# Kernel optimization log

Hardware: AMD Instinct MI355X
Metric: run time of the kernel (lower is better)

Reference implementation:

```python
import jax, jax.numpy as jnp
import numpy as np

V, N, K, D, H = 100000, 20000, 32, 256, 256


def setup_inputs() -> dict:
    key = jax.random.key(0)
    k1, k2, k3, k4, k5, k6 = jax.random.split(key, 6)
    return {
        "embed_table": jax.random.normal(k1, (V, D), dtype=jnp.float32),
        "node_ids": jax.random.randint(k2, (N,), 0, V, dtype=jnp.int64) if jax.config.jax_enable_x64 else jax.random.randint(k2, (N,), 0, V, dtype=jnp.int32),
        "nb_ids": jax.random.randint(k3, (N, K), 0, V, dtype=jnp.int32),
        "self_weight": jax.random.normal(k4, (D, H), dtype=jnp.float32) / np.sqrt(D),
        "nb_weight": jax.random.normal(k5, (D, H), dtype=jnp.float32) / np.sqrt(D),
        "bias": jax.random.normal(k6, (2 * H,), dtype=jnp.float32),
    }


def reference(embed_table, node_ids, nb_ids, self_weight, nb_weight, bias):
    # gather self embeddings: [N, D]
    self_attr = embed_table[node_ids]
    # gather sampled neighbor embeddings [N, K, D] and mean-pool over K
    nb_attr = jnp.mean(embed_table[nb_ids], axis=1)
    from_self = self_attr @ self_weight          # [N, H]
    from_nb = nb_attr @ nb_weight                # [N, H]
    out = jnp.concatenate((from_self, from_nb), axis=1) + bias  # concat combine
    return jax.nn.relu(out)
```

## Files before the change

kernel.cpp:

```cpp
#include <hip/hip_runtime.h>

#define VV 100000
#define NN 20000
#define KK 32
#define DD 256
#define HH 256
#define BN 16

typedef __attribute__((ext_vector_type(8))) short bf16x8;
typedef __attribute__((ext_vector_type(4))) float f32x4;
typedef __attribute__((ext_vector_type(2))) float f32x2;
typedef __attribute__((ext_vector_type(4))) uint  u32x4;
typedef __attribute__((ext_vector_type(2))) uint  u32x2;

__device__ __forceinline__ ushort f2bf(float f) {
    uint u = __float_as_uint(f);
    return (ushort)((u + 0x7FFFu + ((u >> 16) & 1u)) >> 16);
}
__device__ __forceinline__ float bf2f(ushort u) {
    return __uint_as_float(((uint)u) << 16);
}

__global__ __launch_bounds__(256) void k_conv8(
    const float* __restrict__ E, unsigned char* __restrict__ E8)
{
    const size_t i = ((size_t)blockIdx.x * 256 + threadIdx.x) * 16;
    u32x4 o;
    #pragma unroll
    for (int w = 0; w < 4; ++w) {
        const f32x4 a = __builtin_nontemporal_load((const f32x4*)&E[i + w * 4]);
        int r = 0;
        r = __builtin_amdgcn_cvt_pk_fp8_f32(a.x, a.y, r, false);
        r = __builtin_amdgcn_cvt_pk_fp8_f32(a.z, a.w, r, true);
        o[w] = (uint)r;
    }
    *(u32x4*)&E8[i] = o;
}

__global__ __launch_bounds__(256) void k_conv(
    const float* __restrict__ E, ushort* __restrict__ Eb)
{
    const size_t i = ((size_t)blockIdx.x * 256 + threadIdx.x) * 8;
    const f32x4 a = __builtin_nontemporal_load((const f32x4*)&E[i]);
    const f32x4 b = __builtin_nontemporal_load((const f32x4*)&E[i + 4]);
    bf16x8 v;
    v[0] = (short)f2bf(a.x); v[1] = (short)f2bf(a.y);
    v[2] = (short)f2bf(a.z); v[3] = (short)f2bf(a.w);
    v[4] = (short)f2bf(b.x); v[5] = (short)f2bf(b.y);
    v[6] = (short)f2bf(b.z); v[7] = (short)f2bf(b.w);
    *(bf16x8*)&Eb[i] = v;
}

__global__ __launch_bounds__(256) void k_prep_wf(
    const float* __restrict__ Ws, const float* __restrict__ Wn,
    ushort* __restrict__ WTf)
{
    __shared__ float t[256][17];
    const int tid = threadIdx.x;
    const int h   = blockIdx.y;
    const int tt  = blockIdx.x;
    const float* src = h ? Wn : Ws;
    const int h0 = tt * 16;
    const int c = tid & 15, dr = tid >> 4;
    #pragma unroll
    for (int s = 0; s < 16; ++s) {
        const int d = s * 16 + dr;
        t[d][c] = src[(size_t)d * HH + h0 + c];
    }
    __syncthreads();
    const int fl = tid & 63, w = tid >> 6;
    const int r16 = fl & 15, kg = fl >> 4;
    #pragma unroll
    for (int p = 0; p < 2; ++p) {
        const int ks = w + p * 4;
        bf16x8 v;
        #pragma unroll
        for (int e = 0; e < 8; ++e)
            v[e] = (short)f2bf(t[ks * 32 + kg * 8 + e][r16]);
        *(bf16x8*)&WTf[(((size_t)(h * 16 + tt) * 8 + ks) * 64 + fl) * 8] = v;
    }
}

__global__ __launch_bounds__(256) void k_prep_w(
    const float* __restrict__ Ws, const float* __restrict__ Wn,
    ushort* __restrict__ WT)
{
    __shared__ float t[64][65];
    const int tid = threadIdx.x;
    const float* src = (blockIdx.z == 0) ? Ws : Wn;
    ushort* dst = WT + (size_t)blockIdx.z * HH * DD;
    const int d0 = blockIdx.x * 64, h0 = blockIdx.y * 64;

    const int hl = tid & 63, dq = tid >> 6;
    #pragma unroll
    for (int i = 0; i < 16; ++i) {
        const int dl = dq * 16 + i;
        t[dl][hl] = src[(size_t)(d0 + dl) * HH + h0 + hl];
    }
    __syncthreads();
    const int dl = tid & 63, hq = tid >> 6;
    #pragma unroll
    for (int i = 0; i < 16; ++i) {
        const int h2 = hq * 16 + i;
        dst[(size_t)(h0 + h2) * DD + d0 + dl] = f2bf(t[dl][h2]);
    }
}

__global__ __launch_bounds__(256, 6) void k_gather8(
    const float*         __restrict__ Ef,
    const unsigned char* __restrict__ E8,
    const int*           __restrict__ node_ids,
    const int*           __restrict__ nb_ids,
    ushort*              __restrict__ A)
{
    const int wv   = threadIdx.x >> 6;
    const int lane = threadIdx.x & 63;
    const int sub  = lane >> 5, l31 = lane & 31;
    const int g    = blockIdx.x * 4 + wv;
    const int base = g * KK;

    const int srow = node_ids[g];
    const f32x4 s0 = *(const f32x4*)&Ef[(size_t)(uint)srow * DD + l31 * 8];
    const f32x4 s1 = *(const f32x4*)&Ef[(size_t)(uint)srow * DD + l31 * 8 + 4];

    u32x2 d[16];
    #pragma unroll
    for (int j = 0; j < 16; ++j) {
        const int rlo = nb_ids[base + 2 * j];
        const int rhi = nb_ids[base + 2 * j + 1];
        const int row = sub ? rhi : rlo;
        d[j] = *(const u32x2*)&E8[(size_t)(uint)row * DD + l31 * 8];
    }

    float acc[8];
    #pragma unroll
    for (int e = 0; e < 8; ++e) acc[e] = 0.f;
    #pragma unroll
    for (int j = 0; j < 16; ++j) {
        #pragma unroll
        for (int w = 0; w < 2; ++w) {
            const f32x2 lo = __builtin_amdgcn_cvt_pk_f32_fp8((int)d[j][w], false);
            const f32x2 hi = __builtin_amdgcn_cvt_pk_f32_fp8((int)d[j][w], true);
            acc[w * 4 + 0] += lo.x; acc[w * 4 + 1] += lo.y;
            acc[w * 4 + 2] += hi.x; acc[w * 4 + 3] += hi.y;
        }
    }
    #pragma unroll
    for (int e = 0; e < 8; ++e)
        acc[e] += __shfl_xor(acc[e], 32);

    const float inv = 1.0f / (float)KK;
    bf16x8 nv;
    #pragma unroll
    for (int e = 0; e < 8; ++e)
        nv[e] = (short)f2bf(acc[e] * inv);

    bf16x8 sv;
    sv[0] = (short)f2bf(s0.x); sv[1] = (short)f2bf(s0.y);
    sv[2] = (short)f2bf(s0.z); sv[3] = (short)f2bf(s0.w);
    sv[4] = (short)f2bf(s1.x); sv[5] = (short)f2bf(s1.y);
    sv[6] = (short)f2bf(s1.z); sv[7] = (short)f2bf(s1.w);

    const int tile = g >> 4, rr = g & 15;
    const int ks = l31 >> 2, kgw = l31 & 3;
    const size_t dst = (((size_t)(tile * 2 + sub) * 8 + ks) * 64 + kgw * 16 + rr) * 8;
    *(bf16x8*)&A[dst] = sub ? nv : sv;
}

__global__ __launch_bounds__(256, 4) void k_gemmf(
    const ushort* __restrict__ A,
    const ushort* __restrict__ WTf,
    const float*  __restrict__ bias,
    float*        __restrict__ out)
{
    const int wv   = __builtin_amdgcn_readfirstlane((int)(threadIdx.x >> 6));
    const int lane = threadIdx.x & 63;
    const int tile = blockIdx.x;
    const int half = wv >> 1, qt = wv & 1;
    const int r16 = lane & 15, kg = lane >> 4;

    bf16x8 a[8];
    #pragma unroll
    for (int ks = 0; ks < 8; ++ks)
        a[ks] = *(const bf16x8*)&A[(((size_t)(tile * 2 + half) * 8 + ks) * 64 + lane) * 8];

    f32x4 accs[8];
    #pragma unroll
    for (int ct = 0; ct < 8; ++ct) {
        const int t = qt * 8 + ct;
        f32x4 acc = {0.f, 0.f, 0.f, 0.f};
        #pragma unroll
        for (int ks = 0; ks < 8; ++ks) {
            const bf16x8 b = *(const bf16x8*)&WTf[(((size_t)(half * 16 + t) * 8 + ks) * 64 + lane) * 8];
            acc = __builtin_amdgcn_mfma_f32_16x16x32_bf16(a[ks], b, acc, 0, 0, 0);
        }
        accs[ct] = acc;
    }

    #pragma unroll
    for (int ct = 0; ct < 8; ++ct) {
        const int cglob = half * HH + (qt * 8 + ct) * 16 + r16;
        const float bv = bias[cglob];
        #pragma unroll
        for (int r = 0; r < 4; ++r) {
            const float v = accs[ct][r] + bv;
            out[(size_t)(tile * 16 + kg * 4 + r) * (2 * HH) + cglob] = v > 0.f ? v : 0.f;
        }
    }
}

template<int EBF16>
__global__ __launch_bounds__(256, 4) void k_fused(
    const float*  __restrict__ Ef,
    const ushort* __restrict__ Eb,
    const int*    __restrict__ node_ids,
    const int*    __restrict__ nb_ids,
    const ushort* __restrict__ WT,
    const float*  __restrict__ bias,
    float*        __restrict__ out)
{
    __shared__ ushort As[BN][DD];
    __shared__ ushort An[BN][DD];
    const int tid  = threadIdx.x;
    const int wave = tid >> 6;
    const int lane = tid & 63;
    const int g0   = blockIdx.x * BN;

    if (EBF16) {
        const int sub = lane >> 5;
        const int l31 = lane & 31;
        const uint boff = (uint)l31 * 16;
        for (int n = wave; n < BN; n += 4) {
            const int g = g0 + n;
            const int base = g * KK;
            const uint swz = ((uint)(n & 7)) << 4;
            const int srow = node_ids[g];
            const bf16x8 sv = *(const bf16x8*)&Eb[((size_t)(uint)srow << 8) + l31 * 8];
            bf16x8 r[16];
            #pragma unroll
            for (int j = 0; j < 16; ++j) {
                const int rlo = nb_ids[base + 2 * j];
                const int rhi = nb_ids[base + 2 * j + 1];
                const int row = sub ? rhi : rlo;
                r[j] = *(const bf16x8*)&Eb[((size_t)(uint)row << 8) + l31 * 8];
            }
            float acc[8];
            #pragma unroll
            for (int e = 0; e < 8; ++e) acc[e] = 0.f;
            #pragma unroll
            for (int j = 0; j < 16; ++j) {
                #pragma unroll
                for (int e = 0; e < 8; ++e)
                    acc[e] += bf2f((ushort)r[j][e]);
            }
            #pragma unroll
            for (int e = 0; e < 8; ++e)
                acc[e] += __shfl_xor(acc[e], 32);
            const float inv = 1.0f / (float)KK;
            bf16x8 nv;
            #pragma unroll
            for (int e = 0; e < 8; ++e)
                nv[e] = (short)f2bf(acc[e] * inv);
            if (sub == 0) {
                *(bf16x8*)((char*)&As[n][0] + (boff ^ swz)) = sv;
            } else {
                *(bf16x8*)((char*)&An[n][0] + (boff ^ swz)) = nv;
            }
        }
    } else {
        for (int n = wave; n < BN; n += 4) {
            const int g = g0 + n;
            const int srow = node_ids[g];
            const uint swz  = ((uint)(n & 7)) << 4;
            const uint boff = (uint)lane * 8;
            const float4 s = *(const float4*)&Ef[(size_t)srow * DD + lane * 4];
            ushort4 sv = make_ushort4(f2bf(s.x), f2bf(s.y), f2bf(s.z), f2bf(s.w));
            float4 acc = make_float4(0.f, 0.f, 0.f, 0.f);
            #pragma unroll
            for (int k0 = 0; k0 < KK; k0 += 8) {
                float4 r[8];
                #pragma unroll
                for (int j = 0; j < 8; ++j) {
                    const int row = nb_ids[g * KK + k0 + j];
                    r[j] = *(const float4*)&Ef[(size_t)row * DD + lane * 4];
                }
                #pragma unroll
                for (int j = 0; j < 8; ++j) {
                    acc.x += r[j].x; acc.y += r[j].y;
                    acc.z += r[j].z; acc.w += r[j].w;
                }
            }
            const float inv = 1.0f / (float)KK;
            const ushort4 nv = make_ushort4(f2bf(acc.x * inv), f2bf(acc.y * inv),
                                            f2bf(acc.z * inv), f2bf(acc.w * inv));
            *(ushort4*)((char*)&As[n][0] + (boff ^ swz)) = sv;
            *(ushort4*)((char*)&An[n][0] + (boff ^ swz)) = nv;
        }
    }
    __syncthreads();

    const int half = wave >> 1;
    const int colq = (wave & 1) * 128;
    const int r16  = lane & 15;
    const int kg   = lane >> 4;
    const uint rswz = ((uint)(r16 & 7)) << 4;
    const char* Arow = (const char*)(half ? &An[r16][0] : &As[r16][0]);

    bf16x8 a[8];
    #pragma unroll
    for (int ks = 0; ks < 8; ++ks) {
        const uint off = (uint)(ks * 64 + kg * 16);
        a[ks] = *(const bf16x8*)(Arow + (off ^ rswz));
    }

    const ushort* Wb = WT + (size_t)half * HH * DD;
    f32x4 accs[8];
    #pragma unroll
    for (int ct = 0; ct < 8; ++ct) {
        const int c = colq + ct * 16 + r16;
        const ushort* Bb = Wb + (size_t)c * DD + kg * 8;
        f32x4 acc = {0.f, 0.f, 0.f, 0.f};
        #pragma unroll
        for (int ks = 0; ks < 8; ++ks) {
            const bf16x8 b = *(const bf16x8*)(Bb + ks * 32);
            acc = __builtin_amdgcn_mfma_f32_16x16x32_bf16(a[ks], b, acc, 0, 0, 0);
        }
        accs[ct] = acc;
    }

    #pragma unroll
    for (int ct = 0; ct < 8; ++ct) {
        const int cglob = half * HH + colq + ct * 16 + r16;
        const float bv = bias[cglob];
        #pragma unroll
        for (int r = 0; r < 4; ++r) {
            const float v = accs[ct][r] + bv;
            out[(size_t)(g0 + kg * 4 + r) * (2 * HH) + cglob] = v > 0.f ? v : 0.f;
        }
    }
}

__global__ __launch_bounds__(256, 4) void hetegraph_fused_kernel(
    const float* __restrict__ embed, const int* __restrict__ node_ids,
    const int* __restrict__ nb_ids, const float* __restrict__ Ws,
    const float* __restrict__ Wn, const float* __restrict__ bias,
    float* __restrict__ out)
{
    __shared__ float As[BN][DD];
    __shared__ float An[BN][DD];
    const int tid = threadIdx.x, wave = tid >> 6, lane = tid & 63;
    const int g0 = blockIdx.x * BN;
    for (int n = wave; n < BN; n += 4) {
        const int g = g0 + n;
        const int self_row = node_ids[g];
        const float4 s = *(const float4*)&embed[(size_t)self_row * DD + lane * 4];
        float4 acc = make_float4(0.f, 0.f, 0.f, 0.f);
        for (int k0 = 0; k0 < KK; k0 += 8) {
            float4 r[8];
            #pragma unroll
            for (int j = 0; j < 8; ++j) {
                const int row = nb_ids[g * KK + k0 + j];
                r[j] = *(const float4*)&embed[(size_t)row * DD + lane * 4];
            }
            #pragma unroll
            for (int j = 0; j < 8; ++j) {
                acc.x += r[j].x; acc.y += r[j].y; acc.z += r[j].z; acc.w += r[j].w;
            }
        }
        const float inv = 1.0f / (float)KK;
        *(float4*)&As[n][lane * 4] = s;
        float4 m = make_float4(acc.x * inv, acc.y * inv, acc.z * inv, acc.w * inv);
        *(float4*)&An[n][lane * 4] = m;
    }
    __syncthreads();
    const int h = tid;
    {
        float acc[BN];
        #pragma unroll
        for (int n = 0; n < BN; ++n) acc[n] = 0.f;
        for (int d0 = 0; d0 < DD; d0 += 4) {
            const float w0 = Ws[(d0+0)*HH+h], w1 = Ws[(d0+1)*HH+h];
            const float w2 = Ws[(d0+2)*HH+h], w3 = Ws[(d0+3)*HH+h];
            #pragma unroll
            for (int n = 0; n < BN; ++n) {
                const float4 a = *(const float4*)&As[n][d0];
                acc[n] = fmaf(a.x,w0,acc[n]); acc[n] = fmaf(a.y,w1,acc[n]);
                acc[n] = fmaf(a.z,w2,acc[n]); acc[n] = fmaf(a.w,w3,acc[n]);
            }
        }
        const float b = bias[h];
        #pragma unroll
        for (int n = 0; n < BN; ++n) {
            const float v = acc[n] + b;
            out[(size_t)(g0+n)*(2*HH) + h] = v > 0.f ? v : 0.f;
        }
    }
    {
        float acc[BN];
        #pragma unroll
        for (int n = 0; n < BN; ++n) acc[n] = 0.f;
        for (int d0 = 0; d0 < DD; d0 += 4) {
            const float w0 = Wn[(d0+0)*HH+h], w1 = Wn[(d0+1)*HH+h];
            const float w2 = Wn[(d0+2)*HH+h], w3 = Wn[(d0+3)*HH+h];
            #pragma unroll
            for (int n = 0; n < BN; ++n) {
                const float4 a = *(const float4*)&An[n][d0];
                acc[n] = fmaf(a.x,w0,acc[n]); acc[n] = fmaf(a.y,w1,acc[n]);
                acc[n] = fmaf(a.z,w2,acc[n]); acc[n] = fmaf(a.w,w3,acc[n]);
            }
        }
        const float b = bias[HH + h];
        #pragma unroll
        for (int n = 0; n < BN; ++n) {
            const float v = acc[n] + b;
            out[(size_t)(g0+n)*(2*HH) + HH + h] = v > 0.f ? v : 0.f;
        }
    }
}

extern "C" void kernel_launch(void* const* d_in, const int* in_sizes, int n_in,
                              void* d_out, int out_size, void* d_ws, size_t ws_size,
                              hipStream_t stream) {
    const float* embed    = (const float*)d_in[0];
    const int*   node_ids = (const int*)d_in[1];
    const int*   nb_ids   = (const int*)d_in[2];
    const float* Ws       = (const float*)d_in[3];
    const float* Wn       = (const float*)d_in[4];
    const float* bias     = (const float*)d_in[5];
    float*       out      = (float*)d_out;

    const size_t e8_bytes  = (size_t)VV * DD;
    const size_t eb_bytes  = (size_t)VV * DD * sizeof(ushort);
    const size_t wtf_bytes = 2ull * 16 * 8 * 64 * 8 * sizeof(ushort);
    const size_t af_bytes  = (size_t)(NN / 16) * 2 * 8 * 64 * 8 * sizeof(ushort);
    const size_t wt_bytes  = 2ull * HH * DD * sizeof(ushort);

    if (ws_size >= e8_bytes + wtf_bytes + af_bytes) {
        unsigned char* E8  = (unsigned char*)d_ws;
        ushort*        WTf = (ushort*)((char*)d_ws + e8_bytes);
        ushort*        Af  = (ushort*)((char*)d_ws + e8_bytes + wtf_bytes);
        k_prep_wf<<<dim3(16, 2), dim3(256), 0, stream>>>(Ws, Wn, WTf);
        k_conv8<<<dim3(VV * DD / 4096), dim3(256), 0, stream>>>(embed, E8);
        k_gather8<<<dim3(NN / 4), dim3(256), 0, stream>>>(embed, E8, node_ids, nb_ids, Af);
        k_gemmf<<<dim3(NN / 16), dim3(256), 0, stream>>>(Af, WTf, bias, out);
    } else if (ws_size >= eb_bytes + wt_bytes) {
        ushort* Eb = (ushort*)d_ws;
        ushort* WT = (ushort*)((char*)d_ws + eb_bytes);
        k_conv<<<dim3(VV * DD / 2048), dim3(256), 0, stream>>>(embed, Eb);
        k_prep_w<<<dim3(DD / 64, HH / 64, 2), dim3(256), 0, stream>>>(Ws, Wn, WT);
        k_fused<1><<<dim3(NN / BN), dim3(256), 0, stream>>>(
            nullptr, Eb, node_ids, nb_ids, WT, bias, out);
    } else if (ws_size >= wt_bytes) {
        ushort* WT = (ushort*)d_ws;
        k_prep_w<<<dim3(DD / 64, HH / 64, 2), dim3(256), 0, stream>>>(Ws, Wn, WT);
        k_fused<0><<<dim3(NN / BN), dim3(256), 0, stream>>>(
            embed, nullptr, node_ids, nb_ids, WT, bias, out);
    } else {
        hetegraph_fused_kernel<<<dim3(NN / BN), dim3(256), 0, stream>>>(
            embed, node_ids, nb_ids, Ws, Wn, bias, out);
    }
}
```

Baseline: 93.28 us.

## Fuse fp8 gather with GEMM using global_load_lds staging and merged prep kernel

Replaces the four-kernel path (weight prep, fp8 conversion, gather to a workspace A buffer, GEMM) with two kernels. One prep kernel does both the fp8 table conversion and the bf16 weight transpose. A fused kernel then gathers the 32 fp8 neighbor rows per node straight into LDS via global_load_lds, mean-pools them, and runs MFMA against the transposed weights. This removes the intermediate A buffer round trip and one launch, at the cost of more LDS per block (occupancy 3) and a full vmcnt wait before each node's reduction.

```diff
diff --git a/kernel.cpp b/kernel.cpp
--- a/kernel.cpp
+++ b/kernel.cpp
@@ -7,6 +7,12 @@
 #define HH 256
 #define BN 16
 
+#if __has_builtin(__builtin_amdgcn_global_load_lds)
+#define HAS_GLL 1
+#else
+#define HAS_GLL 0
+#endif
+
 typedef __attribute__((ext_vector_type(8))) short bf16x8;
 typedef __attribute__((ext_vector_type(4))) float f32x4;
 typedef __attribute__((ext_vector_type(2))) float f32x2;
@@ -20,6 +26,158 @@
 __device__ __forceinline__ float bf2f(ushort u) {
     return __uint_as_float(((uint)u) << 16);
 }
+
+__global__ __launch_bounds__(256) void k_prep_all(
+    const float* __restrict__ E,  unsigned char* __restrict__ E8,
+    const float* __restrict__ Ws, const float* __restrict__ Wn,
+    ushort* __restrict__ WT)
+{
+    __shared__ float t[64][65];
+    const int tid = threadIdx.x;
+    const int bx  = blockIdx.x;
+
+    if (bx < 6250) {
+        const size_t i = ((size_t)bx * 256 + tid) * 16;
+        u32x4 o;
+        #pragma unroll
+        for (int w = 0; w < 4; ++w) {
+            const f32x4 a = __builtin_nontemporal_load((const f32x4*)&E[i + w * 4]);
+            int r = 0;
+            r = __builtin_amdgcn_cvt_pk_fp8_f32(a.x, a.y, r, false);
+            r = __builtin_amdgcn_cvt_pk_fp8_f32(a.z, a.w, r, true);
+            o[w] = (uint)r;
+        }
+        *(u32x4*)&E8[i] = o;
+        return;
+    }
+
+    const int pb = bx - 6250;
+    const int z  = pb >> 4;
+    const int rem = pb & 15;
+    const int d0 = (rem & 3) * 64, h0 = (rem >> 2) * 64;
+    const float* src = z ? Wn : Ws;
+    ushort* dst = WT + (size_t)z * HH * DD;
+
+    const int hl = tid & 63, dq = tid >> 6;
+    #pragma unroll
+    for (int i = 0; i < 16; ++i) {
+        const int dl = dq * 16 + i;
+        t[dl][hl] = src[(size_t)(d0 + dl) * HH + h0 + hl];
+    }
+    __syncthreads();
+    const int dl = tid & 63, hq = tid >> 6;
+    #pragma unroll
+    for (int i = 0; i < 16; ++i) {
+        const int h2 = hq * 16 + i;
+        dst[(size_t)(h0 + h2) * DD + d0 + dl] = f2bf(t[dl][h2]);
+    }
+}
+
+#if HAS_GLL
+__global__ __launch_bounds__(256, 3) void k_fusedgl(
+    const float*         __restrict__ Ef,
+    const unsigned char* __restrict__ E8,
+    const int*           __restrict__ node_ids,
+    const int*           __restrict__ nb_ids,
+    const ushort*        __restrict__ WT,
+    const float*         __restrict__ bias,
+    float*               __restrict__ out)
+{
+    __shared__ unsigned char stage[4][KK * 256];
+    __shared__ ushort As[BN][DD];
+    __shared__ ushort An[BN][DD];
+    const int tid  = threadIdx.x;
+    const int wv   = tid >> 6;
+    const int lane = tid & 63;
+    const int sub  = lane >> 5, l31 = lane & 31;
+    const int g0   = blockIdx.x * BN;
+
+    for (int it = 0; it < 4; ++it) {
+        const int n = wv + it * 4;
+        const int g = g0 + n;
+        const int base = g * KK;
+
+        const int srow = node_ids[g];
+        const f32x4 s0 = *(const f32x4*)&Ef[(size_t)(uint)srow * DD + l31 * 8];
+        const f32x4 s1 = *(const f32x4*)&Ef[(size_t)(uint)srow * DD + l31 * 8 + 4];
+
+        #pragma unroll
+        for (int j = 0; j < KK; ++j) {
+            const int row = nb_ids[base + j];
+            const unsigned char* gp = E8 + (size_t)(uint)row * DD + lane * 4;
+            __builtin_amdgcn_global_load_lds(
+                (const __attribute__((address_space(1))) void*)gp,
+                (__attribute__((address_space(3))) void*)&stage[wv][j * 256],
+                4, 0, 0);
+        }
+        asm volatile("s_waitcnt vmcnt(0)" ::: "memory");
+        __builtin_amdgcn_sched_barrier(0);
+
+        float a0 = 0.f, a1 = 0.f, a2 = 0.f, a3 = 0.f;
+        #pragma unroll
+        for (int j = 0; j < KK; ++j) {
+            const uint w = *(const uint*)&stage[wv][j * 256 + lane * 4];
+            const f32x2 lo = __builtin_amdgcn_cvt_pk_f32_fp8((int)w, false);
+            const f32x2 hi = __builtin_amdgcn_cvt_pk_f32_fp8((int)w, true);
+            a0 += lo.x; a1 += lo.y; a2 += hi.x; a3 += hi.y;
+        }
+        const float inv = 1.0f / (float)KK;
+        const ushort4 nv = make_ushort4(f2bf(a0 * inv), f2bf(a1 * inv),
+                                        f2bf(a2 * inv), f2bf(a3 * inv));
+        const uint swz = ((uint)(n & 7)) << 4;
+        *(ushort4*)((char*)&An[n][0] + ((((uint)lane) * 8) ^ swz)) = nv;
+        if (sub == 0) {
+            bf16x8 sv;
+            sv[0] = (short)f2bf(s0.x); sv[1] = (short)f2bf(s0.y);
+            sv[2] = (short)f2bf(s0.z); sv[3] = (short)f2bf(s0.w);
+            sv[4] = (short)f2bf(s1.x); sv[5] = (short)f2bf(s1.y);
+            sv[6] = (short)f2bf(s1.z); sv[7] = (short)f2bf(s1.w);
+            *(bf16x8*)((char*)&As[n][0] + ((((uint)l31) * 16) ^ swz)) = sv;
+        }
+    }
+    __syncthreads();
+
+    const int half = wv >> 1;
+    const int colq = (wv & 1) * 128;
+    const int r16  = lane & 15;
+    const int kg   = lane >> 4;
+    const uint rswz = ((uint)(r16 & 7)) << 4;
+    const char* Arow = (const char*)(half ? &An[r16][0] : &As[r16][0]);
+
+    bf16x8 a[8];
+    #pragma unroll
+    for (int ks = 0; ks < 8; ++ks) {
+        const uint off = (uint)(ks * 64 + kg * 16);
+        a[ks] = *(const bf16x8*)(Arow + (off ^ rswz));
+    }
+
+    const ushort* Wb = WT + (size_t)half * HH * DD;
+    f32x4 accs[8];
+    #pragma unroll
+    for (int ct = 0; ct < 8; ++ct) {
+        const int c = colq + ct * 16 + r16;
+        const ushort* Bb = Wb + (size_t)c * DD + kg * 8;
+        f32x4 acc = {0.f, 0.f, 0.f, 0.f};
+        #pragma unroll
+        for (int ks = 0; ks < 8; ++ks) {
+            const bf16x8 b = *(const bf16x8*)(Bb + ks * 32);
+            acc = __builtin_amdgcn_mfma_f32_16x16x32_bf16(a[ks], b, acc, 0, 0, 0);
+        }
+        accs[ct] = acc;
+    }
+
+    #pragma unroll
+    for (int ct = 0; ct < 8; ++ct) {
+        const int cglob = half * HH + colq + ct * 16 + r16;
+        const float bv = bias[cglob];
+        #pragma unroll
+        for (int r = 0; r < 4; ++r) {
+            const float v = accs[ct][r] + bv;
+            out[(size_t)(g0 + kg * 4 + r) * (2 * HH) + cglob] = v > 0.f ? v : 0.f;
+        }
+    }
+}
+#endif
 
 __global__ __launch_bounds__(256) void k_conv8(
     const float* __restrict__ E, unsigned char* __restrict__ E8)
@@ -35,20 +193,6 @@
         o[w] = (uint)r;
     }
     *(u32x4*)&E8[i] = o;
-}
-
-__global__ __launch_bounds__(256) void k_conv(
-    const float* __restrict__ E, ushort* __restrict__ Eb)
-{
-    const size_t i = ((size_t)blockIdx.x * 256 + threadIdx.x) * 8;
-    const f32x4 a = __builtin_nontemporal_load((const f32x4*)&E[i]);
-    const f32x4 b = __builtin_nontemporal_load((const f32x4*)&E[i + 4]);
-    bf16x8 v;
-    v[0] = (short)f2bf(a.x); v[1] = (short)f2bf(a.y);
-    v[2] = (short)f2bf(a.z); v[3] = (short)f2bf(a.w);
-    v[4] = (short)f2bf(b.x); v[5] = (short)f2bf(b.y);
-    v[6] = (short)f2bf(b.z); v[7] = (short)f2bf(b.w);
-    *(bf16x8*)&Eb[i] = v;
 }
 
 __global__ __launch_bounds__(256) void k_prep_wf(
@@ -81,31 +225,6 @@
     }
 }
 
-__global__ __launch_bounds__(256) void k_prep_w(
-    const float* __restrict__ Ws, const float* __restrict__ Wn,
-    ushort* __restrict__ WT)
-{
-    __shared__ float t[64][65];
-    const int tid = threadIdx.x;
-    const float* src = (blockIdx.z == 0) ? Ws : Wn;
-    ushort* dst = WT + (size_t)blockIdx.z * HH * DD;
-    const int d0 = blockIdx.x * 64, h0 = blockIdx.y * 64;
-
-    const int hl = tid & 63, dq = tid >> 6;
-    #pragma unroll
-    for (int i = 0; i < 16; ++i) {
-        const int dl = dq * 16 + i;
-        t[dl][hl] = src[(size_t)(d0 + dl) * HH + h0 + hl];
-    }
-    __syncthreads();
-    const int dl = tid & 63, hq = tid >> 6;
-    #pragma unroll
-    for (int i = 0; i < 16; ++i) {
-        const int h2 = hq * 16 + i;
-        dst[(size_t)(h0 + h2) * DD + d0 + dl] = f2bf(t[dl][h2]);
-    }
-}
-
 __global__ __launch_bounds__(256, 6) void k_gather8(
     const float*         __restrict__ Ef,
     const unsigned char* __restrict__ E8,
@@ -205,137 +324,6 @@
         for (int r = 0; r < 4; ++r) {
             const float v = accs[ct][r] + bv;
             out[(size_t)(tile * 16 + kg * 4 + r) * (2 * HH) + cglob] = v > 0.f ? v : 0.f;
-        }
-    }
-}
-
-template<int EBF16>
-__global__ __launch_bounds__(256, 4) void k_fused(
-    const float*  __restrict__ Ef,
-    const ushort* __restrict__ Eb,
-    const int*    __restrict__ node_ids,
-    const int*    __restrict__ nb_ids,
-    const ushort* __restrict__ WT,
-    const float*  __restrict__ bias,
-    float*        __restrict__ out)
-{
-    __shared__ ushort As[BN][DD];
-    __shared__ ushort An[BN][DD];
-    const int tid  = threadIdx.x;
-    const int wave = tid >> 6;
-    const int lane = tid & 63;
-    const int g0   = blockIdx.x * BN;
-
-    if (EBF16) {
-        const int sub = lane >> 5;
-        const int l31 = lane & 31;
-        const uint boff = (uint)l31 * 16;
-        for (int n = wave; n < BN; n += 4) {
-            const int g = g0 + n;
-            const int base = g * KK;
-            const uint swz = ((uint)(n & 7)) << 4;
-            const int srow = node_ids[g];
-            const bf16x8 sv = *(const bf16x8*)&Eb[((size_t)(uint)srow << 8) + l31 * 8];
-            bf16x8 r[16];
-            #pragma unroll
-            for (int j = 0; j < 16; ++j) {
-                const int rlo = nb_ids[base + 2 * j];
-                const int rhi = nb_ids[base + 2 * j + 1];
-                const int row = sub ? rhi : rlo;
-                r[j] = *(const bf16x8*)&Eb[((size_t)(uint)row << 8) + l31 * 8];
-            }
-            float acc[8];
-            #pragma unroll
-            for (int e = 0; e < 8; ++e) acc[e] = 0.f;
-            #pragma unroll
-            for (int j = 0; j < 16; ++j) {
-                #pragma unroll
-                for (int e = 0; e < 8; ++e)
-                    acc[e] += bf2f((ushort)r[j][e]);
-            }
-            #pragma unroll
-            for (int e = 0; e < 8; ++e)
-                acc[e] += __shfl_xor(acc[e], 32);
-            const float inv = 1.0f / (float)KK;
-            bf16x8 nv;
-            #pragma unroll
-            for (int e = 0; e < 8; ++e)
-                nv[e] = (short)f2bf(acc[e] * inv);
-            if (sub == 0) {
-                *(bf16x8*)((char*)&As[n][0] + (boff ^ swz)) = sv;
-            } else {
-                *(bf16x8*)((char*)&An[n][0] + (boff ^ swz)) = nv;
-            }
-        }
-    } else {
-        for (int n = wave; n < BN; n += 4) {
-            const int g = g0 + n;
-            const int srow = node_ids[g];
-            const uint swz  = ((uint)(n & 7)) << 4;
-            const uint boff = (uint)lane * 8;
-            const float4 s = *(const float4*)&Ef[(size_t)srow * DD + lane * 4];
-            ushort4 sv = make_ushort4(f2bf(s.x), f2bf(s.y), f2bf(s.z), f2bf(s.w));
-            float4 acc = make_float4(0.f, 0.f, 0.f, 0.f);
-            #pragma unroll
-            for (int k0 = 0; k0 < KK; k0 += 8) {
-                float4 r[8];
-                #pragma unroll
-                for (int j = 0; j < 8; ++j) {
-                    const int row = nb_ids[g * KK + k0 + j];
-                    r[j] = *(const float4*)&Ef[(size_t)row * DD + lane * 4];
-                }
-                #pragma unroll
-                for (int j = 0; j < 8; ++j) {
-                    acc.x += r[j].x; acc.y += r[j].y;
-                    acc.z += r[j].z; acc.w += r[j].w;
-                }
-            }
-            const float inv = 1.0f / (float)KK;
-            const ushort4 nv = make_ushort4(f2bf(acc.x * inv), f2bf(acc.y * inv),
-                                            f2bf(acc.z * inv), f2bf(acc.w * inv));
-            *(ushort4*)((char*)&As[n][0] + (boff ^ swz)) = sv;
-            *(ushort4*)((char*)&An[n][0] + (boff ^ swz)) = nv;
-        }
-    }
-    __syncthreads();
-
-    const int half = wave >> 1;
-    const int colq = (wave & 1) * 128;
-    const int r16  = lane & 15;
-    const int kg   = lane >> 4;
-    const uint rswz = ((uint)(r16 & 7)) << 4;
-    const char* Arow = (const char*)(half ? &An[r16][0] : &As[r16][0]);
-
-    bf16x8 a[8];
-    #pragma unroll
-    for (int ks = 0; ks < 8; ++ks) {
-        const uint off = (uint)(ks * 64 + kg * 16);
-        a[ks] = *(const bf16x8*)(Arow + (off ^ rswz));
-    }
-
-    const ushort* Wb = WT + (size_t)half * HH * DD;
-    f32x4 accs[8];
-    #pragma unroll
-    for (int ct = 0; ct < 8; ++ct) {
-        const int c = colq + ct * 16 + r16;
-        const ushort* Bb = Wb + (size_t)c * DD + kg * 8;
-        f32x4 acc = {0.f, 0.f, 0.f, 0.f};
-        #pragma unroll
-        for (int ks = 0; ks < 8; ++ks) {
-            const bf16x8 b = *(const bf16x8*)(Bb + ks * 32);
-            acc = __builtin_amdgcn_mfma_f32_16x16x32_bf16(a[ks], b, acc, 0, 0, 0);
-        }
-        accs[ct] = acc;
-    }
-
-    #pragma unroll
-    for (int ct = 0; ct < 8; ++ct) {
-        const int cglob = half * HH + colq + ct * 16 + r16;
-        const float bv = bias[cglob];
-        #pragma unroll
-        for (int r = 0; r < 4; ++r) {
-            const float v = accs[ct][r] + bv;
-            out[(size_t)(g0 + kg * 4 + r) * (2 * HH) + cglob] = v > 0.f ? v : 0.f;
         }
     }
 }
@@ -430,11 +418,20 @@
     float*       out      = (float*)d_out;
 
     const size_t e8_bytes  = (size_t)VV * DD;
-    const size_t eb_bytes  = (size_t)VV * DD * sizeof(ushort);
+    const size_t wt_bytes  = 2ull * HH * DD * sizeof(ushort);
     const size_t wtf_bytes = 2ull * 16 * 8 * 64 * 8 * sizeof(ushort);
     const size_t af_bytes  = (size_t)(NN / 16) * 2 * 8 * 64 * 8 * sizeof(ushort);
-    const size_t wt_bytes  = 2ull * HH * DD * sizeof(ushort);
-
+
+#if HAS_GLL
+    if (ws_size >= e8_bytes + wt_bytes) {
+        unsigned char* E8 = (unsigned char*)d_ws;
+        ushort*        WT = (ushort*)((char*)d_ws + e8_bytes);
+        k_prep_all<<<dim3(6250 + 32), dim3(256), 0, stream>>>(embed, E8, Ws, Wn, WT);
+        k_fusedgl<<<dim3(NN / BN), dim3(256), 0, stream>>>(
+            embed, E8, node_ids, nb_ids, WT, bias, out);
+        return;
+    }
+#endif
     if (ws_size >= e8_bytes + wtf_bytes + af_bytes) {
         unsigned char* E8  = (unsigned char*)d_ws;
         ushort*        WTf = (ushort*)((char*)d_ws + e8_bytes);
@@ -443,18 +440,6 @@
         k_conv8<<<dim3(VV * DD / 4096), dim3(256), 0, stream>>>(embed, E8);
         k_gather8<<<dim3(NN / 4), dim3(256), 0, stream>>>(embed, E8, node_ids, nb_ids, Af);
         k_gemmf<<<dim3(NN / 16), dim3(256), 0, stream>>>(Af, WTf, bias, out);
-    } else if (ws_size >= eb_bytes + wt_bytes) {
-        ushort* Eb = (ushort*)d_ws;
-        ushort* WT = (ushort*)((char*)d_ws + eb_bytes);
-        k_conv<<<dim3(VV * DD / 2048), dim3(256), 0, stream>>>(embed, Eb);
-        k_prep_w<<<dim3(DD / 64, HH / 64, 2), dim3(256), 0, stream>>>(Ws, Wn, WT);
-        k_fused<1><<<dim3(NN / BN), dim3(256), 0, stream>>>(
-            nullptr, Eb, node_ids, nb_ids, WT, bias, out);
-    } else if (ws_size >= wt_bytes) {
-        ushort* WT = (ushort*)d_ws;
-        k_prep_w<<<dim3(DD / 64, HH / 64, 2), dim3(256), 0, stream>>>(Ws, Wn, WT);
-        k_fused<0><<<dim3(NN / BN), dim3(256), 0, stream>>>(
-            embed, nullptr, node_ids, nb_ids, WT, bias, out);
     } else {
         hetegraph_fused_kernel<<<dim3(NN / BN), dim3(256), 0, stream>>>(
             embed, node_ids, nb_ids, Ws, Wn, bias, out);
```

Result: no change. 93.42 us (+0.1%).
